# Kernel optimization log

Hardware: AMD Instinct MI355X
Metric: run time of the kernel (lower is better)

## Reference

```python
import jax, jax.numpy as jnp
import numpy as np

B, N, M, E, D = 32, 50000, 50000, 1600000, 32


def setup_inputs() -> dict:
    key = jax.random.key(0)
    k1, k2, k3 = jax.random.split(key, 3)
    # COO indices: row 0 = src (in [0,N)), row 1 = dst (in [0,M)); N == M here
    indices = jax.random.randint(k1, (2, E), 0, N, dtype=jnp.int64)
    std = (2.0 / D) ** 0.5  # Kaiming init since d was provided
    values = jax.random.normal(k2, (E,), dtype=jnp.float32) * std
    bias = jnp.zeros((M, 1), dtype=jnp.float32)
    x = jax.random.normal(k3, (B, N, 1), dtype=jnp.float32)
    return {"x": x, "values": values, "bias": bias, "indices": indices}


def reference(x, values, bias, indices):
    # x: (B, N, 1); values: (E,); bias: (M, 1); indices: (2, E)
    src = indices[0]
    dst = indices[1]
    # gather x at src per edge and scale: (B, E)
    contrib = values[None, :] * x[:, src, 0]
    # scatter-add into dst nodes per batch element: (B, M)
    out = jax.vmap(lambda c: jax.ops.segment_sum(c, dst, num_segments=M))(contrib)
    out = out + bias[:, 0][None, :]
    return out[..., None]  # (B, M, 1)
```

## Files before the change

kernel.cpp:

```cpp
#include <hip/hip_runtime.h>


#define BATCH 32
#define DPB   128
#define NB_MAX 400
#define BIN_TPB 1024
#define BIN_CHUNK 4096
#define CAPB  5120
#define CAP   5120

__global__ void k_zero_i32(int* __restrict__ p, int n) {
    const int i = blockIdx.x * blockDim.x + threadIdx.x;
    if (i < n) p[i] = 0;
}

__global__ void k_tx(const float* __restrict__ x, float* __restrict__ xt, int N) {
    __shared__ float tile[32][33];
    const int n0 = blockIdx.x * 32;
    const int tx = threadIdx.x;
    const int ty = threadIdx.y;
    #pragma unroll
    for (int k = 0; k < 4; ++k) {
        const int b = ty + 8 * k;
        const int n = n0 + tx;
        tile[tx][b] = (n < N) ? x[(size_t)b * N + n] : 0.0f;
    }
    __syncthreads();
    #pragma unroll
    for (int k = 0; k < 4; ++k) {
        const int n = n0 + ty + 8 * k;
        if (n < N) xt[(size_t)n * BATCH + tx] = tile[ty + 8 * k][tx];
    }
}

__global__ __launch_bounds__(BIN_TPB) void k_bin(const int* __restrict__ idx,
                                                 const float* __restrict__ values,
                                                 int* __restrict__ gcursor,
                                                 int2* __restrict__ sv,
                                                 int E, int NB) {
    __shared__ int  hist[NB_MAX];
    __shared__ int  loff[NB_MAX];
    __shared__ int  gbase[NB_MAX];
    __shared__ int  gcap[NB_MAX];
    __shared__ int2 svl[BIN_CHUNK];
    __shared__ int  gidx[BIN_CHUNK];
    const int tid = threadIdx.x;
    if (tid < NB) hist[tid] = 0;
    __syncthreads();

    const int c0 = blockIdx.x * BIN_CHUNK;
    const int nE = min(BIN_CHUNK, E - c0);
    const int e0 = c0 + (tid << 2);
    const bool v4 = ((E & 3) == 0) && (e0 + 3 < E);
    int d[4] = {-1, -1, -1, -1};
    if (v4) {
        const int4 d4 = *(const int4*)(idx + E + e0);
        d[0] = d4.x; d[1] = d4.y; d[2] = d4.z; d[3] = d4.w;
    } else {
        #pragma unroll
        for (int k = 0; k < 4; ++k) if (e0 + k < E) d[k] = idx[E + e0 + k];
    }
    #pragma unroll
    for (int k = 0; k < 4; ++k) if (d[k] >= 0) atomicAdd(&hist[d[k] >> 7], 1);
    __syncthreads();
    if (tid < 64) {
        int carry = 0;
        for (int c = 0; c < NB; c += 64) {
            const int j = c + tid;
            const int v = (j < NB) ? hist[j] : 0;
            int inc = v;
            #pragma unroll
            for (int dlt = 1; dlt < 64; dlt <<= 1) {
                const int t = __shfl_up(inc, dlt, 64);
                if (tid >= dlt) inc += t;
            }
            if (j < NB) loff[j] = carry + inc - v;
            carry += __shfl(inc, 63, 64);
        }
    }
    __syncthreads();
    if (tid < NB) {
        const int c = hist[tid];
        if (c) {
            const int old = atomicAdd(&gcursor[tid], c);
            gbase[tid] = tid * CAPB + old;
            gcap[tid]  = CAPB - old;
        } else {
            gbase[tid] = 0;
            gcap[tid]  = 0;
        }
        hist[tid] = 0;
    }
    __syncthreads();
    int   s[4];
    float vv[4];
    if (v4) {
        const int4   s4  = *(const int4*)(idx + e0);
        const float4 v4v = *(const float4*)(values + e0);
        s[0] = s4.x; s[1] = s4.y; s[2] = s4.z; s[3] = s4.w;
        vv[0] = v4v.x; vv[1] = v4v.y; vv[2] = v4v.z; vv[3] = v4v.w;
    } else {
        #pragma unroll
        for (int k = 0; k < 4; ++k) {
            if (e0 + k < E) { s[k] = idx[e0 + k]; vv[k] = values[e0 + k]; }
            else { s[k] = 0; vv[k] = 0.0f; }
        }
    }
    #pragma unroll
    for (int k = 0; k < 4; ++k) {
        if (d[k] >= 0) {
            const int bkt = d[k] >> 7;
            const int off = atomicAdd(&hist[bkt], 1);
            const int slot = loff[bkt] + off;
            const int packed = (s[k] & 0xFFFF) | ((d[k] & 127) << 16);
            svl[slot]  = make_int2(packed, __float_as_int(vv[k]));
            gidx[slot] = (off < gcap[bkt]) ? (gbase[bkt] + off) : -1;
        }
    }
    __syncthreads();
    for (int q = tid; q < nE; q += BIN_TPB) {
        const int gi = gidx[q];
        if (gi >= 0) sv[gi] = svl[q];
    }
}

__global__ __launch_bounds__(1024) void k_sort_gather(const int2* __restrict__ sv,
                                                      const int* __restrict__ gcursor,
                                                      const float* __restrict__ xt,
                                                      const float* __restrict__ bias,
                                                      float* __restrict__ out, int M) {
    __shared__ int2 stage[CAP];
    __shared__ unsigned short perm[CAP];
    __shared__ int cnt[DPB];
    __shared__ int off[DPB + 1];
    __shared__ int cur[DPB];
    __shared__ float tile[DPB][33];

    const int bkt = blockIdx.x;
    const int tid = threadIdx.x;
    const int w    = tid >> 6;
    const int lane = tid & 63;
    const int g    = lane >> 3;
    const int j    = lane & 7;
    const int m0   = bkt * DPB;
    const float4* __restrict__ xt4 = (const float4*)xt;

    const int beg = bkt * CAPB;
    const int end = beg + min(gcursor[bkt], CAPB);

    for (int i = tid; i < DPB * 33; i += 1024) ((float*)tile)[i] = 0.0f;

    for (int t0 = beg; t0 < end; t0 += CAP) {
        const int nE = min(CAP, end - t0);
        __syncthreads();
        if (tid < DPB) cnt[tid] = 0;
        __syncthreads();
        const int head = (t0 & 1);
        if (head && tid == 0) {
            const int2 a = sv[t0];
            stage[0] = a;
            atomicAdd(&cnt[(a.x >> 16) & 127], 1);
        }
        const int npair = (nE - head) >> 1;
        const int4* __restrict__ sv4 = (const int4*)(sv + t0 + head);
        for (int p = tid; p < npair; p += 1024) {
            const int4 q = sv4[p];
            const int i0 = head + (p << 1);
            stage[i0]     = make_int2(q.x, q.y);
            stage[i0 + 1] = make_int2(q.z, q.w);
            atomicAdd(&cnt[(q.x >> 16) & 127], 1);
            atomicAdd(&cnt[(q.z >> 16) & 127], 1);
        }
        if (((nE - head) & 1) && tid == 1023) {
            const int i0 = head + (npair << 1);
            const int2 a = sv[t0 + i0];
            stage[i0] = a;
            atomicAdd(&cnt[(a.x >> 16) & 127], 1);
        }
        __syncthreads();
        if (tid < 64) {
            int carry = 0;
            #pragma unroll
            for (int c = 0; c < DPB; c += 64) {
                const int jj = c + tid;
                const int v = cnt[jj];
                int inc = v;
                #pragma unroll
                for (int dlt = 1; dlt < 64; dlt <<= 1) {
                    const int t = __shfl_up(inc, dlt, 64);
                    if (tid >= dlt) inc += t;
                }
                off[jj] = carry + inc - v;
                cur[jj] = carry + inc - v;
                carry += __shfl(inc, 63, 64);
            }
            if (tid == 0) off[DPB] = carry;
        }
        __syncthreads();
        for (int i = tid; i < nE; i += 1024) {
            const int dl = (stage[i].x >> 16) & 127;
            const int p = atomicAdd(&cur[dl], 1);
            perm[p] = (unsigned short)i;
        }
        __syncthreads();
        #pragma unroll
        for (int k = 0; k < DPB / 16; ++k) {
            const int r  = w + 16 * k;
            const int rb = off[r];
            const int re = off[r + 1];
            float ax = 0.f, ay = 0.f, az = 0.f, aw_ = 0.f;
            float bx = 0.f, by = 0.f, bz = 0.f, bw = 0.f;
            int q = rb;
            for (; q + 15 < re; q += 16) {
                const int2 eA = stage[perm[q + g]];
                const int2 eB = stage[perm[q + 8 + g]];
                const float4 xA = xt4[(size_t)(eA.x & 0xFFFF) * 8 + j];
                const float4 xB = xt4[(size_t)(eB.x & 0xFFFF) * 8 + j];
                const float vA = __int_as_float(eA.y);
                const float vB = __int_as_float(eB.y);
                ax += vA * xA.x; ay += vA * xA.y; az += vA * xA.z; aw_ += vA * xA.w;
                bx += vB * xB.x; by += vB * xB.y; bz += vB * xB.z; bw  += vB * xB.w;
            }
            for (; q < re; q += 8) {
                if (q + g < re) {
                    const int2 e = stage[perm[q + g]];
                    const float4 xv = xt4[(size_t)(e.x & 0xFFFF) * 8 + j];
                    const float v = __int_as_float(e.y);
                    ax += v * xv.x; ay += v * xv.y; az += v * xv.z; aw_ += v * xv.w;
                }
            }
            ax += bx; ay += by; az += bz; aw_ += bw;
            #pragma unroll
            for (int d = 8; d < 64; d <<= 1) {
                ax  += __shfl_xor(ax, d, 64);
                ay  += __shfl_xor(ay, d, 64);
                az  += __shfl_xor(az, d, 64);
                aw_ += __shfl_xor(aw_, d, 64);
            }
            if (g == 0) {
                tile[r][j * 4 + 0] += ax;
                tile[r][j * 4 + 1] += ay;
                tile[r][j * 4 + 2] += az;
                tile[r][j * 4 + 3] += aw_;
            }
        }
    }
    __syncthreads();
    if ((M & 3) == 0) {
        float4* __restrict__ out4 = (float4*)out;
        const float4* __restrict__ bias4 = (const float4*)bias;
        for (int i = tid; i < 32 * (DPB / 4); i += 1024) {
            const int b  = i >> 5;
            const int c4 = i & 31;
            const int m2 = m0 + (c4 << 2);
            if (m2 + 3 < M) {
                const float4 bv = bias4[(m0 >> 2) + c4];
                float4 o;
                o.x = tile[c4 * 4 + 0][b] + bv.x;
                o.y = tile[c4 * 4 + 1][b] + bv.y;
                o.z = tile[c4 * 4 + 2][b] + bv.z;
                o.w = tile[c4 * 4 + 3][b] + bv.w;
                out4[((size_t)b * M + m2) >> 2] = o;
            } else {
                #pragma unroll
                for (int k = 0; k < 4; ++k) {
                    const int m3 = m2 + k;
                    if (m3 < M) out[(size_t)b * M + m3] = tile[c4 * 4 + k][b] + bias[m3];
                }
            }
        }
    } else {
        for (int i = tid; i < 32 * DPB; i += 1024) {
            const int b = i >> 7;
            const int c = i & 127;
            const int m2 = m0 + c;
            if (m2 < M) out[(size_t)b * M + m2] = tile[c][b] + bias[m2];
        }
    }
}

__global__ void k_init_out_t(const float* __restrict__ bias, float* __restrict__ out_t, int M) {
    const int i = blockIdx.x * blockDim.x + threadIdx.x;
    if (i < M * BATCH) out_t[i] = bias[i >> 5];
}

__global__ void k_scatter(const float* __restrict__ xt, const float* __restrict__ values,
                          const int* __restrict__ idx, float* __restrict__ out_t, int E) {
    const int t = blockIdx.x * blockDim.x + threadIdx.x;
    const int e = t >> 5;
    const int b = t & 31;
    if (e < E) {
        const int src = idx[e];
        const int dst = idx[E + e];
        const float contrib = values[e] * xt[(size_t)src * BATCH + b];
        atomicAdd(&out_t[(size_t)dst * BATCH + b], contrib);
    }
}

__global__ void k_transpose_out(const float* __restrict__ out_t, float* __restrict__ out, int M) {
    __shared__ float tile[32][33];
    const int m0 = blockIdx.x * 32;
    const int tx = threadIdx.x;
    const int ty = threadIdx.y;
    #pragma unroll
    for (int k = 0; k < 4; ++k) {
        const int m = m0 + ty + 8 * k;
        if (m < M) tile[ty + 8 * k][tx] = out_t[(size_t)m * BATCH + tx];
    }
    __syncthreads();
    #pragma unroll
    for (int k = 0; k < 4; ++k) {
        const int b = ty + 8 * k;
        const int m = m0 + tx;
        if (m < M) out[(size_t)b * M + m] = tile[tx][b];
    }
}

extern "C" void kernel_launch(void* const* d_in, const int* in_sizes, int n_in,
                              void* d_out, int out_size, void* d_ws, size_t ws_size,
                              hipStream_t stream) {
    const float* x      = (const float*)d_in[0];
    const float* values = (const float*)d_in[1];
    const float* bias   = (const float*)d_in[2];
    const int*   idx    = (const int*)d_in[3];

    const int N = in_sizes[0] / BATCH;
    const int E = in_sizes[3] / 2;
    const int M = in_sizes[2];
    const int NB = (M + DPB - 1) / DPB;

    float* out = (float*)d_out;

    char* base = (char*)d_ws;
    size_t off = 0;
    auto carve = [&](size_t bytes) -> void* {
        void* r = base + off;
        off = (off + bytes + 511) & ~(size_t)511;
        return r;
    };
    float* xt      = (float*)carve((size_t)N * BATCH * sizeof(float));
    float* out_t   = (float*)carve((size_t)M * BATCH * sizeof(float));
    int2*  sv      = (int2*)carve((size_t)NB * CAPB * sizeof(int2));
    int*   gcursor = (int*)carve((size_t)NB * sizeof(int));
    const size_t csr_needed = off;

    dim3 tblk(32, 8);
    const int TB = (N + 31) / 32;

    const bool use_csr = (csr_needed <= ws_size) && (N <= 65536) && (M <= 65536)
                         && (NB <= NB_MAX);
    if (use_csr) {
        k_zero_i32<<<(NB + 255) / 256, 256, 0, stream>>>(gcursor, NB);
        k_tx<<<TB, tblk, 0, stream>>>(x, xt, N);
        k_bin<<<(E + BIN_CHUNK - 1) / BIN_CHUNK, BIN_TPB, 0, stream>>>(idx, values, gcursor, sv, E, NB);
        k_sort_gather<<<NB, 1024, 0, stream>>>(sv, gcursor, xt, bias, out, M);
    } else {
        k_tx<<<TB, tblk, 0, stream>>>(x, xt, N);
        k_init_out_t<<<(M * BATCH + 255) / 256, 256, 0, stream>>>(bias, out_t, M);
        const long long total = (long long)E * BATCH;
        k_scatter<<<(int)((total + 255) / 256), 256, 0, stream>>>(xt, values, idx, out_t, E);
        k_transpose_out<<<(M + 31) / 32, tblk, 0, stream>>>(out_t, out, M);
    }
}
```

Before: 118.9 us.

## Fuse zero, transpose, bin and gather into one cooperative kernel with grid syncs

Replaces the four-kernel pipeline with a single cooperative persistent kernel that runs transpose, binning and sort-gather as phases separated by grid.sync, with NB blocks striding over the work. The goal is to remove launch gaps between kernels. In exchange, binning now runs on only NB blocks instead of one block per chunk, which lowers parallelism in that phase, and grid-wide syncs add their own cost. The kernel falls back to the old path if occupancy cannot hold NB blocks. The odd-alignment head handling in the sort-gather phase was also dropped; this is valid because bucket starts are multiples of CAPB, which is even.

```diff
diff --git a/kernel.cpp b/kernel.cpp
--- a/kernel.cpp
+++ b/kernel.cpp
@@ -1,4 +1,7 @@
 #include <hip/hip_runtime.h>
+#include <hip/hip_cooperative_groups.h>
+
+namespace cg = cooperative_groups;
 
 
 #define BATCH 32
@@ -8,6 +11,288 @@
 #define BIN_CHUNK 4096
 #define CAPB  5120
 #define CAP   5120
+#define SMEM_BYTES 69664
+
+__global__ __launch_bounds__(1024, 8) void k_mega(
+    const float* __restrict__ x, float* __restrict__ xt,
+    const int* __restrict__ idx, const float* __restrict__ values,
+    int* __restrict__ gcursor, int2* __restrict__ sv,
+    const float* __restrict__ bias, float* __restrict__ out,
+    int N, int E, int M, int NB) {
+    __shared__ alignas(16) char smem[SMEM_BYTES];
+    cg::grid_group grid = cg::this_grid();
+    const int tid = threadIdx.x;
+    const int bid = blockIdx.x;
+    const int NG  = gridDim.x;
+
+    {
+        float (*tile)[32][33] = reinterpret_cast<float(*)[32][33]>(smem);
+        if (bid == 0 && tid < NB) gcursor[tid] = 0;
+        const int sub = tid >> 8;
+        const int t2  = tid & 255;
+        const int tx  = t2 & 31;
+        const int ty  = t2 >> 5;
+        const int TBt = (N + 31) / 32;
+        for (int base = bid * 4; base < TBt; base += NG * 4) {
+            const int tb = base + sub;
+            const int n0 = tb * 32;
+            #pragma unroll
+            for (int k = 0; k < 4; ++k) {
+                const int b = ty + 8 * k;
+                const int n = n0 + tx;
+                tile[sub][tx][b] = (tb < TBt && n < N) ? x[(size_t)b * N + n] : 0.0f;
+            }
+            __syncthreads();
+            #pragma unroll
+            for (int k = 0; k < 4; ++k) {
+                const int n = n0 + ty + 8 * k;
+                if (tb < TBt && n < N) xt[(size_t)n * BATCH + tx] = tile[sub][ty + 8 * k][tx];
+            }
+            __syncthreads();
+        }
+    }
+    __threadfence();
+    grid.sync();
+    __threadfence();
+
+    {
+        int*  hist  = (int*)(smem);
+        int*  loff  = (int*)(smem + 1600);
+        int*  gbase = (int*)(smem + 3200);
+        int*  gcap  = (int*)(smem + 4800);
+        int2* svl   = (int2*)(smem + 6400);
+        int*  gidx  = (int*)(smem + 39168);
+        const int nchunks = (E + BIN_CHUNK - 1) / BIN_CHUNK;
+        for (int ch = bid; ch < nchunks; ch += NG) {
+            const int c0 = ch * BIN_CHUNK;
+            const int nE = min(BIN_CHUNK, E - c0);
+            if (tid < NB) hist[tid] = 0;
+            __syncthreads();
+            const int e0 = c0 + (tid << 2);
+            const bool v4 = ((E & 3) == 0) && (e0 + 3 < E);
+            int d[4] = {-1, -1, -1, -1};
+            if (v4) {
+                const int4 d4 = *(const int4*)(idx + E + e0);
+                d[0] = d4.x; d[1] = d4.y; d[2] = d4.z; d[3] = d4.w;
+            } else {
+                #pragma unroll
+                for (int k = 0; k < 4; ++k) if (e0 + k < E) d[k] = idx[E + e0 + k];
+            }
+            #pragma unroll
+            for (int k = 0; k < 4; ++k) if (d[k] >= 0) atomicAdd(&hist[d[k] >> 7], 1);
+            __syncthreads();
+            if (tid < 64) {
+                int carry = 0;
+                for (int c = 0; c < NB; c += 64) {
+                    const int j = c + tid;
+                    const int v = (j < NB) ? hist[j] : 0;
+                    int inc = v;
+                    #pragma unroll
+                    for (int dlt = 1; dlt < 64; dlt <<= 1) {
+                        const int t = __shfl_up(inc, dlt, 64);
+                        if (tid >= dlt) inc += t;
+                    }
+                    if (j < NB) loff[j] = carry + inc - v;
+                    carry += __shfl(inc, 63, 64);
+                }
+            }
+            __syncthreads();
+            if (tid < NB) {
+                const int c = hist[tid];
+                if (c) {
+                    const int old = atomicAdd(&gcursor[tid], c);
+                    gbase[tid] = tid * CAPB + old;
+                    gcap[tid]  = CAPB - old;
+                } else {
+                    gbase[tid] = 0;
+                    gcap[tid]  = 0;
+                }
+                hist[tid] = 0;
+            }
+            __syncthreads();
+            int   s[4];
+            float vv[4];
+            if (v4) {
+                const int4   s4  = *(const int4*)(idx + e0);
+                const float4 v4v = *(const float4*)(values + e0);
+                s[0] = s4.x; s[1] = s4.y; s[2] = s4.z; s[3] = s4.w;
+                vv[0] = v4v.x; vv[1] = v4v.y; vv[2] = v4v.z; vv[3] = v4v.w;
+            } else {
+                #pragma unroll
+                for (int k = 0; k < 4; ++k) {
+                    if (e0 + k < E) { s[k] = idx[e0 + k]; vv[k] = values[e0 + k]; }
+                    else { s[k] = 0; vv[k] = 0.0f; }
+                }
+            }
+            #pragma unroll
+            for (int k = 0; k < 4; ++k) {
+                if (d[k] >= 0) {
+                    const int bkt = d[k] >> 7;
+                    const int off = atomicAdd(&hist[bkt], 1);
+                    const int slot = loff[bkt] + off;
+                    const int packed = (s[k] & 0xFFFF) | ((d[k] & 127) << 16);
+                    svl[slot]  = make_int2(packed, __float_as_int(vv[k]));
+                    gidx[slot] = (off < gcap[bkt]) ? (gbase[bkt] + off) : -1;
+                }
+            }
+            __syncthreads();
+            for (int q = tid; q < nE; q += BIN_TPB) {
+                const int gi = gidx[q];
+                if (gi >= 0) sv[gi] = svl[q];
+            }
+            __syncthreads();
+        }
+    }
+    __threadfence();
+    grid.sync();
+    __threadfence();
+
+    {
+        int2* stage = (int2*)(smem);
+        unsigned short* perm = (unsigned short*)(smem + 40960);
+        int* cnt = (int*)(smem + 51200);
+        int* off = (int*)(smem + 51712);
+        int* cur = (int*)(smem + 52232);
+        float (*tile)[33] = (float(*)[33])(smem + 52744);
+
+        const int w    = tid >> 6;
+        const int lane = tid & 63;
+        const int g    = lane >> 3;
+        const int j    = lane & 7;
+        const float4* __restrict__ xt4 = (const float4*)xt;
+
+        for (int bkt = bid; bkt < NB; bkt += NG) {
+            const int m0  = bkt * DPB;
+            const int beg = bkt * CAPB;
+            const int end = beg + min(gcursor[bkt], CAPB);
+
+            for (int i = tid; i < DPB * 33; i += 1024) ((float*)tile)[i] = 0.0f;
+
+            for (int t0 = beg; t0 < end; t0 += CAP) {
+                const int nE = min(CAP, end - t0);
+                __syncthreads();
+                if (tid < DPB) cnt[tid] = 0;
+                __syncthreads();
+                const int npair = nE >> 1;
+                const int4* __restrict__ sv4 = (const int4*)(sv + t0);
+                for (int p = tid; p < npair; p += 1024) {
+                    const int4 q = sv4[p];
+                    const int i0 = p << 1;
+                    stage[i0]     = make_int2(q.x, q.y);
+                    stage[i0 + 1] = make_int2(q.z, q.w);
+                    atomicAdd(&cnt[(q.x >> 16) & 127], 1);
+                    atomicAdd(&cnt[(q.z >> 16) & 127], 1);
+                }
+                if ((nE & 1) && tid == 1023) {
+                    const int i0 = npair << 1;
+                    const int2 a = sv[t0 + i0];
+                    stage[i0] = a;
+                    atomicAdd(&cnt[(a.x >> 16) & 127], 1);
+                }
+                __syncthreads();
+                if (tid < 64) {
+                    int carry = 0;
+                    #pragma unroll
+                    for (int c = 0; c < DPB; c += 64) {
+                        const int jj = c + tid;
+                        const int v = cnt[jj];
+                        int inc = v;
+                        #pragma unroll
+                        for (int dlt = 1; dlt < 64; dlt <<= 1) {
+                            const int t = __shfl_up(inc, dlt, 64);
+                            if (tid >= dlt) inc += t;
+                        }
+                        off[jj] = carry + inc - v;
+                        cur[jj] = carry + inc - v;
+                        carry += __shfl(inc, 63, 64);
+                    }
+                    if (tid == 0) off[DPB] = carry;
+                }
+                __syncthreads();
+                for (int i = tid; i < nE; i += 1024) {
+                    const int dl = (stage[i].x >> 16) & 127;
+                    const int p = atomicAdd(&cur[dl], 1);
+                    perm[p] = (unsigned short)i;
+                }
+                __syncthreads();
+                #pragma unroll
+                for (int k = 0; k < DPB / 16; ++k) {
+                    const int r  = w + 16 * k;
+                    const int rb = off[r];
+                    const int re = off[r + 1];
+                    float ax = 0.f, ay = 0.f, az = 0.f, aw_ = 0.f;
+                    float bx = 0.f, by = 0.f, bz = 0.f, bw = 0.f;
+                    int q = rb;
+                    for (; q + 15 < re; q += 16) {
+                        const int2 eA = stage[perm[q + g]];
+                        const int2 eB = stage[perm[q + 8 + g]];
+                        const float4 xA = xt4[(size_t)(eA.x & 0xFFFF) * 8 + j];
+                        const float4 xB = xt4[(size_t)(eB.x & 0xFFFF) * 8 + j];
+                        const float vA = __int_as_float(eA.y);
+                        const float vB = __int_as_float(eB.y);
+                        ax += vA * xA.x; ay += vA * xA.y; az += vA * xA.z; aw_ += vA * xA.w;
+                        bx += vB * xB.x; by += vB * xB.y; bz += vB * xB.z; bw  += vB * xB.w;
+                    }
+                    for (; q < re; q += 8) {
+                        if (q + g < re) {
+                            const int2 e = stage[perm[q + g]];
+                            const float4 xv = xt4[(size_t)(e.x & 0xFFFF) * 8 + j];
+                            const float v = __int_as_float(e.y);
+                            ax += v * xv.x; ay += v * xv.y; az += v * xv.z; aw_ += v * xv.w;
+                        }
+                    }
+                    ax += bx; ay += by; az += bz; aw_ += bw;
+                    #pragma unroll
+                    for (int d = 8; d < 64; d <<= 1) {
+                        ax  += __shfl_xor(ax, d, 64);
+                        ay  += __shfl_xor(ay, d, 64);
+                        az  += __shfl_xor(az, d, 64);
+                        aw_ += __shfl_xor(aw_, d, 64);
+                    }
+                    if (g == 0) {
+                        tile[r][j * 4 + 0] += ax;
+                        tile[r][j * 4 + 1] += ay;
+                        tile[r][j * 4 + 2] += az;
+                        tile[r][j * 4 + 3] += aw_;
+                    }
+                }
+            }
+            __syncthreads();
+            if ((M & 3) == 0) {
+                float4* __restrict__ out4 = (float4*)out;
+                const float4* __restrict__ bias4 = (const float4*)bias;
+                for (int i = tid; i < 32 * (DPB / 4); i += 1024) {
+                    const int b  = i >> 5;
+                    const int c4 = i & 31;
+                    const int m2 = m0 + (c4 << 2);
+                    if (m2 + 3 < M) {
+                        const float4 bv = bias4[(m0 >> 2) + c4];
+                        float4 o;
+                        o.x = tile[c4 * 4 + 0][b] + bv.x;
+                        o.y = tile[c4 * 4 + 1][b] + bv.y;
+                        o.z = tile[c4 * 4 + 2][b] + bv.z;
+                        o.w = tile[c4 * 4 + 3][b] + bv.w;
+                        out4[((size_t)b * M + m2) >> 2] = o;
+                    } else {
+                        #pragma unroll
+                        for (int k = 0; k < 4; ++k) {
+                            const int m3 = m2 + k;
+                            if (m3 < M) out[(size_t)b * M + m3] = tile[c4 * 4 + k][b] + bias[m3];
+                        }
+                    }
+                }
+            } else {
+                for (int i = tid; i < 32 * DPB; i += 1024) {
+                    const int b = i >> 7;
+                    const int c = i & 127;
+                    const int m2 = m0 + c;
+                    if (m2 < M) out[(size_t)b * M + m2] = tile[c][b] + bias[m2];
+                }
+            }
+            __syncthreads();
+        }
+    }
+}
 
 __global__ void k_zero_i32(int* __restrict__ p, int n) {
     const int i = blockIdx.x * blockDim.x + threadIdx.x;
@@ -47,7 +332,6 @@
     const int tid = threadIdx.x;
     if (tid < NB) hist[tid] = 0;
     __syncthreads();
-
     const int c0 = blockIdx.x * BIN_CHUNK;
     const int nE = min(BIN_CHUNK, E - c0);
     const int e0 = c0 + (tid << 2);
@@ -135,7 +419,6 @@
     __shared__ int off[DPB + 1];
     __shared__ int cur[DPB];
     __shared__ float tile[DPB][33];
-
     const int bkt = blockIdx.x;
     const int tid = threadIdx.x;
     const int w    = tid >> 6;
@@ -144,35 +427,26 @@
     const int j    = lane & 7;
     const int m0   = bkt * DPB;
     const float4* __restrict__ xt4 = (const float4*)xt;
-
     const int beg = bkt * CAPB;
     const int end = beg + min(gcursor[bkt], CAPB);
-
     for (int i = tid; i < DPB * 33; i += 1024) ((float*)tile)[i] = 0.0f;
-
     for (int t0 = beg; t0 < end; t0 += CAP) {
         const int nE = min(CAP, end - t0);
         __syncthreads();
         if (tid < DPB) cnt[tid] = 0;
         __syncthreads();
-        const int head = (t0 & 1);
-        if (head && tid == 0) {
-            const int2 a = sv[t0];
-            stage[0] = a;
-            atomicAdd(&cnt[(a.x >> 16) & 127], 1);
-        }
-        const int npair = (nE - head) >> 1;
-        const int4* __restrict__ sv4 = (const int4*)(sv + t0 + head);
+        const int npair = nE >> 1;
+        const int4* __restrict__ sv4 = (const int4*)(sv + t0);
         for (int p = tid; p < npair; p += 1024) {
             const int4 q = sv4[p];
-            const int i0 = head + (p << 1);
+            const int i0 = p << 1;
             stage[i0]     = make_int2(q.x, q.y);
             stage[i0 + 1] = make_int2(q.z, q.w);
             atomicAdd(&cnt[(q.x >> 16) & 127], 1);
             atomicAdd(&cnt[(q.z >> 16) & 127], 1);
         }
-        if (((nE - head) & 1) && tid == 1023) {
-            const int i0 = head + (npair << 1);
+        if ((nE & 1) && tid == 1023) {
+            const int i0 = npair << 1;
             const int2 a = sv[t0 + i0];
             stage[i0] = a;
             atomicAdd(&cnt[(a.x >> 16) & 127], 1);
@@ -349,11 +623,34 @@
 
     const bool use_csr = (csr_needed <= ws_size) && (N <= 65536) && (M <= 65536)
                          && (NB <= NB_MAX);
+
     if (use_csr) {
-        k_zero_i32<<<(NB + 255) / 256, 256, 0, stream>>>(gcursor, NB);
-        k_tx<<<TB, tblk, 0, stream>>>(x, xt, N);
-        k_bin<<<(E + BIN_CHUNK - 1) / BIN_CHUNK, BIN_TPB, 0, stream>>>(idx, values, gcursor, sv, E, NB);
-        k_sort_gather<<<NB, 1024, 0, stream>>>(sv, gcursor, xt, bias, out, M);
+        static int s_capacity = -1;
+        if (s_capacity < 0) {
+            int nbk = 0, ncu = 0, dev = 0;
+            hipError_t e0 = hipGetDevice(&dev);
+            hipError_t e1 = hipOccupancyMaxActiveBlocksPerMultiprocessor(&nbk, k_mega, 1024, 0);
+            hipError_t e2 = hipDeviceGetAttribute(&ncu, hipDeviceAttributeMultiprocessorCount, dev);
+            s_capacity = (e0 == hipSuccess && e1 == hipSuccess && e2 == hipSuccess)
+                         ? nbk * ncu : 0;
+        }
+        const int NG = NB;
+        bool launched = false;
+        if (s_capacity >= NG) {
+            int Nv = N, Ev = E, Mv = M, NBv = NB;
+            void* args[] = {(void*)&x, (void*)&xt, (void*)&idx, (void*)&values,
+                            (void*)&gcursor, (void*)&sv, (void*)&bias, (void*)&out,
+                            (void*)&Nv, (void*)&Ev, (void*)&Mv, (void*)&NBv};
+            hipError_t err = hipLaunchCooperativeKernel(k_mega, dim3(NG), dim3(1024),
+                                                        args, 0, stream);
+            launched = (err == hipSuccess);
+        }
+        if (!launched) {
+            k_zero_i32<<<(NB + 255) / 256, 256, 0, stream>>>(gcursor, NB);
+            k_tx<<<TB, tblk, 0, stream>>>(x, xt, N);
+            k_bin<<<(E + BIN_CHUNK - 1) / BIN_CHUNK, BIN_TPB, 0, stream>>>(idx, values, gcursor, sv, E, NB);
+            k_sort_gather<<<NB, 1024, 0, stream>>>(sv, gcursor, xt, bias, out, M);
+        }
     } else {
         k_tx<<<TB, tblk, 0, stream>>>(x, xt, N);
         k_init_out_t<<<(M * BATCH + 255) / 256, 256, 0, stream>>>(bias, out_t, M);
```

Result: no change. 119.7 us (+0.7%).
